# Optimization experiments

Measured on AMD Instinct MI355X. Metric: run time of the kernel, lower is better.

The kernel has to match this reference:

```python
import jax, jax.numpy as jnp
import numpy as np

# Grouped masked GEMM dims (see DeepSeekMOE._up_gate/_down):
# G = num_experts // ep = 8; M = m_per_group = 32
# up/gate: k = hidden_size = 4096, n = 2*expert_dim = 2816
# down   : k = expert_dim  = 1408, n = hidden_size = 4096
G, M = 8, 32
K_UG, N_UG = 4096, 2816
K_DN, N_DN = 1408, 4096


def setup_inputs() -> dict:
    key = jax.random.key(0)
    k1, k2, k3, k4, k5 = jax.random.split(key, 5)
    x_ug = jax.random.normal(k1, (G, M, K_UG), dtype=jnp.float32)
    w_ug = jax.random.normal(k2, (G, N_UG, K_UG), dtype=jnp.float32) * 0.02  # NT layout [g, n, k]
    x_dn = jax.random.normal(k3, (G, M, K_DN), dtype=jnp.float32)
    w_dn = jax.random.normal(k4, (G, N_DN, K_DN), dtype=jnp.float32) * 0.02  # NT layout [g, n, k]
    masked_m = jax.random.randint(k5, (G,), 0, M, dtype=jnp.int32)  # per-group valid row count
    return {"x_ug": x_ug, "w_ug": w_ug, "x_dn": x_dn, "w_dn": w_dn, "masked_m": masked_m}


def reference(x_ug, w_ug, x_dn, w_dn, masked_m):
    # Row-validity mask: rows >= masked_m[g] are skipped by the masked grouped GEMM
    # (their output is zero / undefined; we define it as zero).
    row = jnp.arange(M, dtype=jnp.int32)
    mask = (row[None, :] < masked_m[:, None])[:, :, None]  # [G, M, 1]

    # Masked grouped GEMM, NT layout: out[g] = x[g] @ w[g].T on valid rows.
    out_ug = jnp.einsum('gmk,gnk->gmn', x_ug, w_ug)  # [G, M, N_UG]  up/gate proj
    out_dn = jnp.einsum('gmk,gnk->gmn', x_dn, w_dn)  # [G, M, N_DN]  down proj

    out_ug = jnp.where(mask, out_ug, jnp.zeros((), out_ug.dtype))
    out_dn = jnp.where(mask, out_dn, jnp.zeros((), out_dn.dtype))
    # Pack both grouped-GEMM outputs into one array along the feature dim.
    return jnp.concatenate([out_ug, out_dn], axis=-1)  # [G, M, N_UG + N_DN]
```

## Files before the change

kernel.cpp:

```cpp
#include <hip/hip_runtime.h>


#define G_    8
#define M_    32
#define KUG   4096
#define NUG   2816
#define KDN   1408
#define NDN   4096
#define NOUT  (NUG + NDN)
#define BN    64
#define BK    64
#define NBUP  (G_ * (NUG / BN))
#define NBDN  (G_ * (NDN / BN))

typedef __attribute__((ext_vector_type(8))) short  bf16x8;
typedef __attribute__((ext_vector_type(4))) float  f32x4;

typedef __attribute__((address_space(3))) float        lds_f32;
typedef const __attribute__((address_space(1))) float  gbl_f32;

__device__ __forceinline__ short f2bf(float x) {
  unsigned u = __float_as_uint(x);
  u = u + 0x7fffu + ((u >> 16) & 1u);
  return (short)(u >> 16);
}

__device__ __forceinline__ bf16x8 cvt_frag(const float* p) {
  f32x4 lo = *(const f32x4*)p;
  f32x4 hi = *(const f32x4*)(p + 4);
  bf16x8 o;
#pragma unroll
  for (int j = 0; j < 4; ++j) { o[j] = f2bf(lo[j]); o[4 + j] = f2bf(hi[j]); }
  return o;
}

__device__ __forceinline__ void stage(float* dst, const float* wg, const float* xg,
                                      int K, int k0, int t) {
#pragma unroll
  for (int rr = 0; rr < 4; ++rr) {
    int gr  = rr * 256 + t;
    int row = gr >> 4;
    int col = (gr & 15) << 2;
    __builtin_amdgcn_global_load_lds((gbl_f32*)(wg + (size_t)row * K + k0 + col),
                                     (lds_f32*)(dst + gr * 4), 16, 0, 0);
  }
#pragma unroll
  for (int rr = 0; rr < 2; ++rr) {
    int gr  = rr * 256 + t;
    int row = gr >> 4;
    int col = (gr & 15) << 2;
    __builtin_amdgcn_global_load_lds((gbl_f32*)(xg + (size_t)row * K + k0 + col),
                                     (lds_f32*)(dst + 4096 + gr * 4), 16, 0, 0);
  }
}

__global__ __launch_bounds__(256, 3) void moe_masked_gemm(
    const float* __restrict__ x_ug, const float* __restrict__ w_ug,
    const float* __restrict__ x_dn, const float* __restrict__ w_dn,
    const int* __restrict__ masked_m, float* __restrict__ out) {
  __shared__ float lds[2][64 * 64 + 32 * 64];

  int b = blockIdx.x;
  const float* xg;
  const float* wg;
  int K, NIT, g, nb, colOff;
  if (b < NBUP) {
    g = b / 44; nb = b - g * 44;
    K = KUG; NIT = KUG / BK; colOff = 0;
    wg = w_ug + ((size_t)g * NUG + (size_t)nb * BN) * KUG;
    xg = x_ug + (size_t)g * M_ * KUG;
  } else {
    int b2 = b - NBUP;
    g = b2 >> 6; nb = b2 & 63;
    K = KDN; NIT = KDN / BK; colOff = NUG;
    wg = w_dn + ((size_t)g * NDN + (size_t)nb * BN) * KDN;
    xg = x_dn + (size_t)g * M_ * KDN;
  }

  int t  = threadIdx.x;
  int mm = masked_m[g];
  float* outg = out + (size_t)g * M_ * NOUT + colOff + (size_t)nb * BN;

  if (mm == 0) {
#pragma unroll
    for (int i = 0; i < 8; ++i) {
      int e = i * 256 + t;
      outg[(size_t)(e >> 6) * NOUT + (e & 63)] = 0.f;
    }
    return;
  }

  int lane = t & 63, wv = t >> 6;
  int r = lane & 15, kb = lane >> 4;

  f32x4 acc0 = {0.f, 0.f, 0.f, 0.f};
  f32x4 acc1 = {0.f, 0.f, 0.f, 0.f};

  stage(&lds[0][0], wg, xg, K, 0, t);
  __syncthreads();

  int cur = 0;
  for (int it = 0; it < NIT; ++it) {
    if (it + 1 < NIT) stage(&lds[cur ^ 1][0], wg, xg, K, (it + 1) * BK, t);

    const float* Ws = &lds[cur][0];
    const float* Xs = Ws + 64 * 64;
#pragma unroll
    for (int kc = 0; kc < 2; ++kc) {
      int ko = kc * 32 + kb * 8;
      bf16x8 a0 = cvt_frag(Xs + r * 64 + ko);
      bf16x8 a1 = cvt_frag(Xs + (r + 16) * 64 + ko);
      bf16x8 bb = cvt_frag(Ws + (wv * 16 + r) * 64 + ko);
      acc0 = __builtin_amdgcn_mfma_f32_16x16x32_bf16(a0, bb, acc0, 0, 0, 0);
      acc1 = __builtin_amdgcn_mfma_f32_16x16x32_bf16(a1, bb, acc1, 0, 0, 0);
    }
    __syncthreads();
    cur ^= 1;
  }

  float* op = outg + wv * 16 + r;
  int m0 = kb * 4;
#pragma unroll
  for (int i = 0; i < 4; ++i) {
    op[(size_t)(m0 + i) * NOUT]      = (m0 + i      < mm) ? acc0[i] : 0.f;
    op[(size_t)(m0 + i + 16) * NOUT] = (m0 + i + 16 < mm) ? acc1[i] : 0.f;
  }
}

extern "C" void kernel_launch(void* const* d_in, const int* in_sizes, int n_in,
                              void* d_out, int out_size, void* d_ws, size_t ws_size,
                              hipStream_t stream) {
  const float* x_ug     = (const float*)d_in[0];
  const float* w_ug     = (const float*)d_in[1];
  const float* x_dn     = (const float*)d_in[2];
  const float* w_dn     = (const float*)d_in[3];
  const int*   masked_m = (const int*)d_in[4];
  float*       out      = (float*)d_out;

  moe_masked_gemm<<<dim3(NBUP + NBDN), dim3(256), 0, stream>>>(
      x_ug, w_ug, x_dn, w_dn, masked_m, out);
}
```

Baseline: 132.7 us.

## Swizzle LDS layout, use packed bf16 convert, interleave up/down block order

The staging step now XOR-swizzles the 16-byte column chunks by row, and the fragment reads apply the same swizzle, so that LDS reads from the 16 rows hit fewer bank conflicts. The manual round-to-nearest bf16 conversion is replaced with the hardware v_cvt_pk_bf16_f32 instruction, which packs two values per instruction. Block indices are remapped so that up/gate blocks (long K) and down blocks (short K) are interleaved 11:16 across the grid, to balance load per CU. The cost is a little extra index arithmetic and reliance on inline asm for the convert.

```diff
diff --git a/kernel.cpp b/kernel.cpp
--- a/kernel.cpp
+++ b/kernel.cpp
@@ -13,25 +13,30 @@
 #define NBUP  (G_ * (NUG / BN))
 #define NBDN  (G_ * (NDN / BN))
 
-typedef __attribute__((ext_vector_type(8))) short  bf16x8;
-typedef __attribute__((ext_vector_type(4))) float  f32x4;
+typedef __attribute__((ext_vector_type(8))) short    bf16x8;
+typedef __attribute__((ext_vector_type(4))) float    f32x4;
+typedef __attribute__((ext_vector_type(4))) unsigned u32x4;
 
 typedef __attribute__((address_space(3))) float        lds_f32;
 typedef const __attribute__((address_space(1))) float  gbl_f32;
 
-__device__ __forceinline__ short f2bf(float x) {
-  unsigned u = __float_as_uint(x);
-  u = u + 0x7fffu + ((u >> 16) & 1u);
-  return (short)(u >> 16);
+union Frag { u32x4 u; bf16x8 s; };
+
+__device__ __forceinline__ unsigned cvtpk(float lo, float hi) {
+  unsigned r;
+  asm("v_cvt_pk_bf16_f32 %0, %1, %2" : "=v"(r) : "v"(lo), "v"(hi));
+  return r;
 }
 
-__device__ __forceinline__ bf16x8 cvt_frag(const float* p) {
-  f32x4 lo = *(const f32x4*)p;
-  f32x4 hi = *(const f32x4*)(p + 4);
-  bf16x8 o;
-#pragma unroll
-  for (int j = 0; j < 4; ++j) { o[j] = f2bf(lo[j]); o[4 + j] = f2bf(hi[j]); }
-  return o;
+__device__ __forceinline__ bf16x8 cvt_frag(const float* row, int G, int s) {
+  f32x4 lo = *(const f32x4*)(row + (((G)     ^ s) << 2));
+  f32x4 hi = *(const f32x4*)(row + (((G + 1) ^ s) << 2));
+  Frag f;
+  f.u[0] = cvtpk(lo[0], lo[1]);
+  f.u[1] = cvtpk(lo[2], lo[3]);
+  f.u[2] = cvtpk(hi[0], hi[1]);
+  f.u[3] = cvtpk(hi[2], hi[3]);
+  return f.s;
 }
 
 __device__ __forceinline__ void stage(float* dst, const float* wg, const float* xg,
@@ -40,7 +45,7 @@
   for (int rr = 0; rr < 4; ++rr) {
     int gr  = rr * 256 + t;
     int row = gr >> 4;
-    int col = (gr & 15) << 2;
+    int col = ((gr & 15) ^ (row & 7)) << 2;
     __builtin_amdgcn_global_load_lds((gbl_f32*)(wg + (size_t)row * K + k0 + col),
                                      (lds_f32*)(dst + gr * 4), 16, 0, 0);
   }
@@ -48,7 +53,7 @@
   for (int rr = 0; rr < 2; ++rr) {
     int gr  = rr * 256 + t;
     int row = gr >> 4;
-    int col = (gr & 15) << 2;
+    int col = ((gr & 15) ^ (row & 7)) << 2;
     __builtin_amdgcn_global_load_lds((gbl_f32*)(xg + (size_t)row * K + k0 + col),
                                      (lds_f32*)(dst + 4096 + gr * 4), 16, 0, 0);
   }
@@ -60,7 +65,10 @@
     const int* __restrict__ masked_m, float* __restrict__ out) {
   __shared__ float lds[2][64 * 64 + 32 * 64];
 
-  int b = blockIdx.x;
+  int p = blockIdx.x;
+  int period = p / 27, slot = p - period * 27;
+  int b = (slot < 11) ? (period * 11 + slot) : (NBUP + period * 16 + (slot - 11));
+
   const float* xg;
   const float* wg;
   int K, NIT, g, nb, colOff;
@@ -92,6 +100,7 @@
 
   int lane = t & 63, wv = t >> 6;
   int r = lane & 15, kb = lane >> 4;
+  int s = r & 7;
 
   f32x4 acc0 = {0.f, 0.f, 0.f, 0.f};
   f32x4 acc1 = {0.f, 0.f, 0.f, 0.f};
@@ -107,10 +116,10 @@
     const float* Xs = Ws + 64 * 64;
 #pragma unroll
     for (int kc = 0; kc < 2; ++kc) {
-      int ko = kc * 32 + kb * 8;
-      bf16x8 a0 = cvt_frag(Xs + r * 64 + ko);
-      bf16x8 a1 = cvt_frag(Xs + (r + 16) * 64 + ko);
-      bf16x8 bb = cvt_frag(Ws + (wv * 16 + r) * 64 + ko);
+      int G = kc * 8 + kb * 2;
+      bf16x8 a0 = cvt_frag(Xs + r * 64,              G, s);
+      bf16x8 a1 = cvt_frag(Xs + (r + 16) * 64,       G, s);
+      bf16x8 bb = cvt_frag(Ws + (wv * 16 + r) * 64,  G, s);
       acc0 = __builtin_amdgcn_mfma_f32_16x16x32_bf16(a0, bb, acc0, 0, 0, 0);
       acc1 = __builtin_amdgcn_mfma_f32_16x16x32_bf16(a1, bb, acc1, 0, 0, 0);
     }
```

Measured after the change: 140.9 us. +6.2%, slower.

## Triple-buffer LDS with vmcnt waits, XOR swizzle, and interleave up/down blocks

Applied to the files above, without the earlier changes.

Replaces the double-buffered LDS pipeline with a three-stage ring that prefetches two tiles ahead. It synchronizes with explicit s_waitcnt vmcnt plus a single s_barrier per iteration instead of two __syncthreads. Staged columns are XOR-swizzled by row to reduce LDS bank conflicts on the fragment reads. Block indices are remapped so up-proj and down-proj blocks interleave in an 11:16 ratio, and the float-to-bf16 conversion now uses the HIP intrinsic. The larger LDS footprint lowers occupancy to two blocks per SM, and the hand-written wait counts depend on exactly six async loads per stage.

```diff
diff --git a/kernel.cpp b/kernel.cpp
--- a/kernel.cpp
+++ b/kernel.cpp
@@ -1,4 +1,5 @@
 #include <hip/hip_runtime.h>
+#include <hip/hip_bf16.h>
 
 
 #define G_    8
@@ -12,22 +13,26 @@
 #define BK    64
 #define NBUP  (G_ * (NUG / BN))
 #define NBDN  (G_ * (NDN / BN))
+#define TILEF (64 * 64 + 32 * 64)
 
-typedef __attribute__((ext_vector_type(8))) short  bf16x8;
-typedef __attribute__((ext_vector_type(4))) float  f32x4;
+typedef __attribute__((ext_vector_type(8))) short    bf16x8;
+typedef __attribute__((ext_vector_type(4))) float    f32x4;
 
 typedef __attribute__((address_space(3))) float        lds_f32;
 typedef const __attribute__((address_space(1))) float  gbl_f32;
 
+#define ASM_BARRIER()   asm volatile("s_barrier" ::: "memory")
+#define VMCNT(n)        asm volatile("s_waitcnt vmcnt(" #n ")" ::: "memory")
+
 __device__ __forceinline__ short f2bf(float x) {
-  unsigned u = __float_as_uint(x);
-  u = u + 0x7fffu + ((u >> 16) & 1u);
-  return (short)(u >> 16);
+  union { __hip_bfloat16 h; short s; } u;
+  u.h = __hip_bfloat16(x);
+  return u.s;
 }
 
-__device__ __forceinline__ bf16x8 cvt_frag(const float* p) {
-  f32x4 lo = *(const f32x4*)p;
-  f32x4 hi = *(const f32x4*)(p + 4);
+__device__ __forceinline__ bf16x8 cvt_frag(const float* row, int Gr, int s) {
+  f32x4 lo = *(const f32x4*)(row + (((Gr)     ^ s) << 2));
+  f32x4 hi = *(const f32x4*)(row + (((Gr + 1) ^ s) << 2));
   bf16x8 o;
 #pragma unroll
   for (int j = 0; j < 4; ++j) { o[j] = f2bf(lo[j]); o[4 + j] = f2bf(hi[j]); }
@@ -40,7 +45,7 @@
   for (int rr = 0; rr < 4; ++rr) {
     int gr  = rr * 256 + t;
     int row = gr >> 4;
-    int col = (gr & 15) << 2;
+    int col = ((gr & 15) ^ (row & 7)) << 2;
     __builtin_amdgcn_global_load_lds((gbl_f32*)(wg + (size_t)row * K + k0 + col),
                                      (lds_f32*)(dst + gr * 4), 16, 0, 0);
   }
@@ -48,19 +53,22 @@
   for (int rr = 0; rr < 2; ++rr) {
     int gr  = rr * 256 + t;
     int row = gr >> 4;
-    int col = (gr & 15) << 2;
+    int col = ((gr & 15) ^ (row & 7)) << 2;
     __builtin_amdgcn_global_load_lds((gbl_f32*)(xg + (size_t)row * K + k0 + col),
                                      (lds_f32*)(dst + 4096 + gr * 4), 16, 0, 0);
   }
 }
 
-__global__ __launch_bounds__(256, 3) void moe_masked_gemm(
+__global__ __launch_bounds__(256, 2) void moe_masked_gemm(
     const float* __restrict__ x_ug, const float* __restrict__ w_ug,
     const float* __restrict__ x_dn, const float* __restrict__ w_dn,
     const int* __restrict__ masked_m, float* __restrict__ out) {
-  __shared__ float lds[2][64 * 64 + 32 * 64];
+  __shared__ float lds[3][TILEF];
 
-  int b = blockIdx.x;
+  int p = blockIdx.x;
+  int period = p / 27, slot = p - period * 27;
+  int b = (slot < 11) ? (period * 11 + slot) : (NBUP + period * 16 + (slot - 11));
+
   const float* xg;
   const float* wg;
   int K, NIT, g, nb, colOff;
@@ -92,30 +100,37 @@
 
   int lane = t & 63, wv = t >> 6;
   int r = lane & 15, kb = lane >> 4;
+  int s = r & 7;
 
   f32x4 acc0 = {0.f, 0.f, 0.f, 0.f};
   f32x4 acc1 = {0.f, 0.f, 0.f, 0.f};
 
   stage(&lds[0][0], wg, xg, K, 0, t);
-  __syncthreads();
+  if (NIT > 1) stage(&lds[1][0], wg, xg, K, BK, t);
 
   int cur = 0;
   for (int it = 0; it < NIT; ++it) {
-    if (it + 1 < NIT) stage(&lds[cur ^ 1][0], wg, xg, K, (it + 1) * BK, t);
+    if (it + 1 < NIT) { VMCNT(6); } else { VMCNT(0); }
+    ASM_BARRIER();
+
+    if (it + 2 < NIT) {
+      int nx = cur + 2; if (nx >= 3) nx -= 3;
+      stage(&lds[nx][0], wg, xg, K, (it + 2) * BK, t);
+    }
 
     const float* Ws = &lds[cur][0];
     const float* Xs = Ws + 64 * 64;
 #pragma unroll
     for (int kc = 0; kc < 2; ++kc) {
-      int ko = kc * 32 + kb * 8;
-      bf16x8 a0 = cvt_frag(Xs + r * 64 + ko);
-      bf16x8 a1 = cvt_frag(Xs + (r + 16) * 64 + ko);
-      bf16x8 bb = cvt_frag(Ws + (wv * 16 + r) * 64 + ko);
+      int Gr = kc * 8 + kb * 2;
+      bf16x8 a0 = cvt_frag(Xs + r * 64,             Gr, s);
+      bf16x8 a1 = cvt_frag(Xs + (r + 16) * 64,      Gr, s);
+      bf16x8 bb = cvt_frag(Ws + (wv * 16 + r) * 64, Gr, s);
       acc0 = __builtin_amdgcn_mfma_f32_16x16x32_bf16(a0, bb, acc0, 0, 0, 0);
       acc1 = __builtin_amdgcn_mfma_f32_16x16x32_bf16(a1, bb, acc1, 0, 0, 0);
     }
-    __syncthreads();
-    cur ^= 1;
+
+    cur += 1; if (cur >= 3) cur -= 3;
   }
 
   float* op = outg + wv * 16 + r;
```

New measurement: 136.7 us. 3.0% more time.

## Replace LDS-staged 256-thread GEMM with single-wave register-pipelined 32x32 tiles

Applied to the files above, without the earlier changes.

Replaces the 256-thread block that staged W and X tiles through LDS with global_load_lds and synchronised each k-step with single-wavefront blocks. Each block now computes a 32x32 output tile, loading fragments straight from global memory into registers with a manual two-stage software pipeline, and drops LDS and barriers entirely. Blocks are interleaved by group for load balance, and bf16 conversion uses the hip_bf16 intrinsic. This removes sync and LDS traffic and gives many more blocks, but each block re-reads X from global/L2 and loads are strided per lane, so coalescing and X reuse across N tiles depend on cache.

```diff
diff --git a/kernel.cpp b/kernel.cpp
--- a/kernel.cpp
+++ b/kernel.cpp
@@ -1,4 +1,5 @@
 #include <hip/hip_runtime.h>
+#include <hip/hip_bf16.h>
 
 
 #define G_    8
@@ -8,122 +9,107 @@
 #define KDN   1408
 #define NDN   4096
 #define NOUT  (NUG + NDN)
-#define BN    64
-#define BK    64
-#define NBUP  (G_ * (NUG / BN))
-#define NBDN  (G_ * (NDN / BN))
+#define UPT   (NUG / 32)
+#define DNT   (NDN / 32)
+#define UPG   (UPT + DNT)
 
-typedef __attribute__((ext_vector_type(8))) short  bf16x8;
-typedef __attribute__((ext_vector_type(4))) float  f32x4;
-
-typedef __attribute__((address_space(3))) float        lds_f32;
-typedef const __attribute__((address_space(1))) float  gbl_f32;
+typedef __attribute__((ext_vector_type(8))) short bf16x8;
+typedef __attribute__((ext_vector_type(4))) float f32x4;
 
 __device__ __forceinline__ short f2bf(float x) {
-  unsigned u = __float_as_uint(x);
-  u = u + 0x7fffu + ((u >> 16) & 1u);
-  return (short)(u >> 16);
+  union { __hip_bfloat16 h; short s; } u;
+  u.h = __hip_bfloat16(x);
+  return u.s;
 }
 
-__device__ __forceinline__ bf16x8 cvt_frag(const float* p) {
-  f32x4 lo = *(const f32x4*)p;
-  f32x4 hi = *(const f32x4*)(p + 4);
+__device__ __forceinline__ bf16x8 cvt8(f32x4 lo, f32x4 hi) {
   bf16x8 o;
 #pragma unroll
   for (int j = 0; j < 4; ++j) { o[j] = f2bf(lo[j]); o[4 + j] = f2bf(hi[j]); }
   return o;
 }
 
-__device__ __forceinline__ void stage(float* dst, const float* wg, const float* xg,
-                                      int K, int k0, int t) {
-#pragma unroll
-  for (int rr = 0; rr < 4; ++rr) {
-    int gr  = rr * 256 + t;
-    int row = gr >> 4;
-    int col = (gr & 15) << 2;
-    __builtin_amdgcn_global_load_lds((gbl_f32*)(wg + (size_t)row * K + k0 + col),
-                                     (lds_f32*)(dst + gr * 4), 16, 0, 0);
-  }
-#pragma unroll
-  for (int rr = 0; rr < 2; ++rr) {
-    int gr  = rr * 256 + t;
-    int row = gr >> 4;
-    int col = (gr & 15) << 2;
-    __builtin_amdgcn_global_load_lds((gbl_f32*)(xg + (size_t)row * K + k0 + col),
-                                     (lds_f32*)(dst + 4096 + gr * 4), 16, 0, 0);
-  }
-}
+#define LOADST(W, X, k0)                                        \
+  do {                                                          \
+    W[0][0] = *(const f32x4*)(wp0 + (k0));                      \
+    W[0][1] = *(const f32x4*)(wp0 + (k0) + 4);                  \
+    W[1][0] = *(const f32x4*)(wp1 + (k0));                      \
+    W[1][1] = *(const f32x4*)(wp1 + (k0) + 4);                  \
+    X[0][0] = *(const f32x4*)(xp0 + (k0));                      \
+    X[0][1] = *(const f32x4*)(xp0 + (k0) + 4);                  \
+    X[1][0] = *(const f32x4*)(xp1 + (k0));                      \
+    X[1][1] = *(const f32x4*)(xp1 + (k0) + 4);                  \
+  } while (0)
 
-__global__ __launch_bounds__(256, 3) void moe_masked_gemm(
+#define COMPST(W, X)                                                      \
+  do {                                                                    \
+    bf16x8 a0 = cvt8(X[0][0], X[0][1]);                                   \
+    bf16x8 a1 = cvt8(X[1][0], X[1][1]);                                   \
+    bf16x8 b0 = cvt8(W[0][0], W[0][1]);                                   \
+    bf16x8 b1 = cvt8(W[1][0], W[1][1]);                                   \
+    acc00 = __builtin_amdgcn_mfma_f32_16x16x32_bf16(a0, b0, acc00, 0, 0, 0); \
+    acc01 = __builtin_amdgcn_mfma_f32_16x16x32_bf16(a0, b1, acc01, 0, 0, 0); \
+    acc10 = __builtin_amdgcn_mfma_f32_16x16x32_bf16(a1, b0, acc10, 0, 0, 0); \
+    acc11 = __builtin_amdgcn_mfma_f32_16x16x32_bf16(a1, b1, acc11, 0, 0, 0); \
+  } while (0)
+
+__global__ __launch_bounds__(64, 4) void moe_masked_gemm(
     const float* __restrict__ x_ug, const float* __restrict__ w_ug,
     const float* __restrict__ x_dn, const float* __restrict__ w_dn,
     const int* __restrict__ masked_m, float* __restrict__ out) {
-  __shared__ float lds[2][64 * 64 + 32 * 64];
+  int b = blockIdx.x;
+  int g = b & 7;
+  int u = b >> 3;
 
-  int b = blockIdx.x;
+  const float* wg;
   const float* xg;
-  const float* wg;
-  int K, NIT, g, nb, colOff;
-  if (b < NBUP) {
-    g = b / 44; nb = b - g * 44;
-    K = KUG; NIT = KUG / BK; colOff = 0;
-    wg = w_ug + ((size_t)g * NUG + (size_t)nb * BN) * KUG;
+  int K, NIT, n0, colOff;
+  if (u < UPT) {
+    K = KUG; NIT = KUG / 32; n0 = u * 32; colOff = 0;
+    wg = w_ug + ((size_t)g * NUG + n0) * KUG;
     xg = x_ug + (size_t)g * M_ * KUG;
   } else {
-    int b2 = b - NBUP;
-    g = b2 >> 6; nb = b2 & 63;
-    K = KDN; NIT = KDN / BK; colOff = NUG;
-    wg = w_dn + ((size_t)g * NDN + (size_t)nb * BN) * KDN;
+    int ud = u - UPT;
+    K = KDN; NIT = KDN / 32; n0 = ud * 32; colOff = NUG;
+    wg = w_dn + ((size_t)g * NDN + n0) * KDN;
     xg = x_dn + (size_t)g * M_ * KDN;
   }
 
-  int t  = threadIdx.x;
   int mm = masked_m[g];
-  float* outg = out + (size_t)g * M_ * NOUT + colOff + (size_t)nb * BN;
+  int t = threadIdx.x, r = t & 15, q = t >> 4;
 
-  if (mm == 0) {
-#pragma unroll
-    for (int i = 0; i < 8; ++i) {
-      int e = i * 256 + t;
-      outg[(size_t)(e >> 6) * NOUT + (e & 63)] = 0.f;
+  const float* wp0 = wg + (size_t)r * K + q * 8;
+  const float* wp1 = wp0 + (size_t)16 * K;
+  const float* xp0 = xg + (size_t)r * K + q * 8;
+  const float* xp1 = xp0 + (size_t)16 * K;
+
+  f32x4 acc00 = {0.f, 0.f, 0.f, 0.f}, acc01 = {0.f, 0.f, 0.f, 0.f};
+  f32x4 acc10 = {0.f, 0.f, 0.f, 0.f}, acc11 = {0.f, 0.f, 0.f, 0.f};
+
+  if (mm != 0) {
+    f32x4 wa[2][2], xa[2][2], wb[2][2], xb[2][2];
+    LOADST(wa, xa, 0);
+    int it = 0;
+    for (; it + 2 < NIT; it += 2) {
+      LOADST(wb, xb, (it + 1) * 32);
+      COMPST(wa, xa);
+      LOADST(wa, xa, (it + 2) * 32);
+      COMPST(wb, xb);
     }
-    return;
+    LOADST(wb, xb, (NIT - 1) * 32);
+    COMPST(wa, xa);
+    COMPST(wb, xb);
   }
 
-  int lane = t & 63, wv = t >> 6;
-  int r = lane & 15, kb = lane >> 4;
-
-  f32x4 acc0 = {0.f, 0.f, 0.f, 0.f};
-  f32x4 acc1 = {0.f, 0.f, 0.f, 0.f};
-
-  stage(&lds[0][0], wg, xg, K, 0, t);
-  __syncthreads();
-
-  int cur = 0;
-  for (int it = 0; it < NIT; ++it) {
-    if (it + 1 < NIT) stage(&lds[cur ^ 1][0], wg, xg, K, (it + 1) * BK, t);
-
-    const float* Ws = &lds[cur][0];
-    const float* Xs = Ws + 64 * 64;
-#pragma unroll
-    for (int kc = 0; kc < 2; ++kc) {
-      int ko = kc * 32 + kb * 8;
-      bf16x8 a0 = cvt_frag(Xs + r * 64 + ko);
-      bf16x8 a1 = cvt_frag(Xs + (r + 16) * 64 + ko);
-      bf16x8 bb = cvt_frag(Ws + (wv * 16 + r) * 64 + ko);
-      acc0 = __builtin_amdgcn_mfma_f32_16x16x32_bf16(a0, bb, acc0, 0, 0, 0);
-      acc1 = __builtin_amdgcn_mfma_f32_16x16x32_bf16(a1, bb, acc1, 0, 0, 0);
-    }
-    __syncthreads();
-    cur ^= 1;
-  }
-
-  float* op = outg + wv * 16 + r;
-  int m0 = kb * 4;
+  float* outg = out + (size_t)g * M_ * NOUT + colOff + n0;
 #pragma unroll
   for (int i = 0; i < 4; ++i) {
-    op[(size_t)(m0 + i) * NOUT]      = (m0 + i      < mm) ? acc0[i] : 0.f;
-    op[(size_t)(m0 + i + 16) * NOUT] = (m0 + i + 16 < mm) ? acc1[i] : 0.f;
+    int m0 = q * 4 + i;
+    int m1 = 16 + m0;
+    outg[(size_t)m0 * NOUT + r]      = (m0 < mm) ? acc00[i] : 0.f;
+    outg[(size_t)m0 * NOUT + 16 + r] = (m0 < mm) ? acc01[i] : 0.f;
+    outg[(size_t)m1 * NOUT + r]      = (m1 < mm) ? acc10[i] : 0.f;
+    outg[(size_t)m1 * NOUT + 16 + r] = (m1 < mm) ? acc11[i] : 0.f;
   }
 }
 
@@ -137,6 +123,6 @@
   const int*   masked_m = (const int*)d_in[4];
   float*       out      = (float*)d_out;
 
-  moe_masked_gemm<<<dim3(NBUP + NBDN), dim3(256), 0, stream>>>(
+  moe_masked_gemm<<<dim3(G_ * UPG), dim3(64), 0, stream>>>(
       x_ug, w_ug, x_dn, w_dn, masked_m, out);
 }
```

Result: slower. 147.3 us (+11.0%).
